# Performance work log

Measured on AMD Instinct MI355X. Metric: run time of the kernel, lower is better.

## Reference

```python
import jax, jax.numpy as jnp
import numpy as np

B, D, N_TYPES = 512, 768, 16
MARGIN = 1.0


def setup_inputs() -> dict:
    key = jax.random.key(0)
    k1, k2 = jax.random.split(key)
    entity_types = jax.random.randint(k1, (B,), 0, N_TYPES, dtype=jnp.int64)
    embeddings = jax.random.normal(k2, (B, D), dtype=jnp.float32)
    return {"entity_types": entity_types, "embeddings": embeddings}


def _pairwise_l2(x):
    # Euclidean distance matrix [B, B], matching torch.cdist(x, x, p=2)
    sq_norm = jnp.sum(x * x, axis=-1)  # [B]
    sq = sq_norm[:, None] + sq_norm[None, :] - 2.0 * (x @ x.T)
    sq = jnp.maximum(sq, 0.0)
    # safe sqrt: zero gradient where sq == 0 (diagonal)
    return jnp.where(sq > 0, jnp.sqrt(jnp.where(sq > 0, sq, 1.0)), 0.0)


def reference(entity_types, embeddings):
    # type_coherence[i, j] = (type_i == type_j)
    type_coherence = entity_types[:, None] == entity_types[None, :]  # [B, B]
    # valid_triplets[a, p, n] = same_type(a, p) & different_type(a, n)
    valid_triplets = type_coherence[:, :, None] & (~type_coherence)[:, None, :]  # [B, B, B]
    distances = _pairwise_l2(embeddings)  # [B, B]
    # triplet_distances[a, p, n] = (d[a, p] - d[a, n]) masked by validity
    triplet_distances = (distances[:, :, None] - distances[:, None, :]) * valid_triplets
    # NOTE: faithful to original — margin added to ALL B^3 entries before clamp,
    # so each invalid triplet contributes clamp(margin, 0) = margin to the sum.
    loss = jnp.sum(jnp.maximum(triplet_distances + MARGIN, 0.0))
    return loss / jnp.sum(valid_triplets)
```

## Files before the change

### kernel.cpp

```cpp
#include <hip/hip_runtime.h>
#include <hip/hip_bf16.h>

#define BSZ 512
#define DIM 768
#define NTYPES 16
#define MARGIN 1.0f
#define PITCH 776

typedef short bf16x8 __attribute__((ext_vector_type(8)));
typedef float f32x4 __attribute__((ext_vector_type(4)));


__global__ __launch_bounds__(256) void gram_kernel(
    const float* __restrict__ emb,
    float* __restrict__ G,
    float* __restrict__ nrm,
    float* __restrict__ out)
{
    const int tid = threadIdx.x;
    const int blk = blockIdx.x;
    const int ti = blk >> 4, tj = blk & 15;
    const int i0 = ti * 32, j0 = tj * 32;

    if (blk == 0 && tid == 0) out[0] = 0.f;

    __shared__ ushort sR[64][PITCH];

    #pragma unroll 12
    for (int it = 0; it < 48; ++it) {
        const int flat = it * 256 + tid;
        const int row = flat / 192;
        const int c4 = flat - row * 192;
        const int grow = (row < 32) ? (i0 + row) : (j0 + row - 32);
        const float4 v = *(const float4*)(emb + (size_t)grow * DIM + c4 * 4);
        __hip_bfloat162 h0 = __float22bfloat162_rn(make_float2(v.x, v.y));
        __hip_bfloat162 h1 = __float22bfloat162_rn(make_float2(v.z, v.w));
        unsigned u0, u1;
        __builtin_memcpy(&u0, &h0, 4);
        __builtin_memcpy(&u1, &h1, 4);
        *(uint2*)&sR[row][c4 * 4] = make_uint2(u0, u1);
    }
    __syncthreads();

    const int lane = tid & 63;
    const int w = tid >> 6;
    const int wr = w >> 1, wc = w & 1;
    const int m = lane & 15;
    const int q = lane >> 4;

    const ushort* arow = &sR[wr * 16 + m][q * 8];
    const ushort* brow = &sR[32 + wc * 16 + m][q * 8];

    f32x4 acc_e = {0.f, 0.f, 0.f, 0.f};
    f32x4 acc_o = {0.f, 0.f, 0.f, 0.f};
    #pragma unroll
    for (int kc = 0; kc < 24; kc += 2) {
        const bf16x8 ae = *(const bf16x8*)(arow + kc * 32);
        const bf16x8 be = *(const bf16x8*)(brow + kc * 32);
        const bf16x8 ao = *(const bf16x8*)(arow + kc * 32 + 32);
        const bf16x8 bo = *(const bf16x8*)(brow + kc * 32 + 32);
        acc_e = __builtin_amdgcn_mfma_f32_16x16x32_bf16(ae, be, acc_e, 0, 0, 0);
        acc_o = __builtin_amdgcn_mfma_f32_16x16x32_bf16(ao, bo, acc_o, 0, 0, 0);
    }

    const int gi = i0 + wr * 16 + 4 * q;
    const int gj = j0 + wc * 16 + m;
    float res[4];
    #pragma unroll
    for (int r = 0; r < 4; ++r) {
        res[r] = acc_e[r] + acc_o[r];
        G[(size_t)(gi + r) * BSZ + gj] = res[r];
    }
    if (ti == tj && wr == wc && (m >> 2) == q)
        nrm[i0 + wr * 16 + m] = res[m & 3];
}

__global__ __launch_bounds__(256) void triplet_kernel(
    const float* __restrict__ G, const float* __restrict__ nrm,
    const int* __restrict__ types, float* __restrict__ out)
{
    const int a = blockIdx.x;
    const int tid = threadIdx.x;
    const int lane = tid & 63;
    const int w = tid >> 6;

    __shared__ float snrm[BSZ];
    __shared__ int   stypes[BSZ];
    __shared__ float pos[BSZ], neg[BSZ];
    __shared__ int   npos, nneg, cnt[NTYPES];
    __shared__ float wsum[4];

    if (tid == 0) { npos = 0; nneg = 0; }
    if (tid < NTYPES) cnt[tid] = 0;
    for (int j = tid; j < BSZ; j += 256) { stypes[j] = types[j]; snrm[j] = nrm[j]; }
    __syncthreads();

    const int ta = stypes[a];
    const float na = snrm[a];
    for (int j = tid; j < BSZ; j += 256) atomicAdd(&cnt[stypes[j]], 1);

    #pragma unroll
    for (int jj = 0; jj < 2; ++jj) {
        const int j = jj * 256 + tid;
        const float g = G[(size_t)a * BSZ + j];
        const float d = sqrtf(fmaxf(na + snrm[j] - 2.f * g, 0.f));
        const bool isp = (stypes[j] == ta);
        const unsigned long long mm = __ballot(isp);
        const unsigned long long below = mm & ((1ull << lane) - 1ull);
        const int cp = __popcll(mm);
        int basep = 0, basen = 0;
        if (lane == 0) {
            basep = atomicAdd(&npos, cp);
            basen = atomicAdd(&nneg, 64 - cp);
        }
        basep = __shfl(basep, 0);
        basen = __shfl(basen, 0);
        const int pb = (int)__popcll(below);
        if (isp) pos[basep + pb] = d;
        else     neg[basen + (lane - pb)] = d;
    }
    __syncthreads();
    const int np = npos, nn = nneg;

    float nr[8];
    #pragma unroll
    for (int c = 0; c < 8; ++c) {
        const int n = c * 64 + lane;
        nr[c] = (n < nn) ? neg[n] : 3.0e38f;
    }
    float local = 0.f;
    for (int pi = w; pi < np; pi += 4) {
        const float dpm = pos[pi] + MARGIN;
        #pragma unroll
        for (int c = 0; c < 8; ++c)
            local += fmaxf(dpm - nr[c], 0.f);
    }

    #pragma unroll
    for (int off = 32; off > 0; off >>= 1) local += __shfl_down(local, off);
    if (lane == 0) wsum[w] = local;
    __syncthreads();
    if (tid == 0) {
        long long V = 0;
        #pragma unroll
        for (int t = 0; t < NTYPES; ++t) {
            long long c = cnt[t];
            V += c * c * (long long)(BSZ - c);
        }
        double bs = (double)wsum[0] + (double)wsum[1]
                  + (double)wsum[2] + (double)wsum[3];
        float contrib = (float)(bs / (double)V);
        if (a == 0) {
            const long long B3 = (long long)BSZ * BSZ * BSZ;
            contrib += (float)((double)(B3 - V) * (double)MARGIN / (double)V);
        }
        atomicAdd(out, contrib);
    }
}

extern "C" void kernel_launch(void* const* d_in, const int* in_sizes, int n_in,
                              void* d_out, int out_size, void* d_ws, size_t ws_size,
                              hipStream_t stream) {
    const int* types = (const int*)d_in[0];
    const float* emb = (const float*)d_in[1];
    float* out = (float*)d_out;

    float* G = (float*)d_ws;
    float* nrm = G + (size_t)BSZ * BSZ;

    gram_kernel<<<256, 256, 0, stream>>>(emb, G, nrm, out);
    triplet_kernel<<<BSZ, 256, 0, stream>>>(G, nrm, types, out);
}
```

Measured before the change: 71.07 us.

## Split-K gram across 8 waves and fuse norm and sqrt into gram kernel

The gram kernel now launches 512 threads and splits the K dimension across two wave groups, which combine their partial sums through shared memory. It computes fp32 row norms while loading the tile and writes the final distance matrix directly, so the separate norm array and the per-element sqrt in the triplet kernel go away. The triplet kernel also issues its distance loads before shared-memory setup to hide their latency. The cost is an extra barrier and shared-memory reduction, and the norms are now computed in fp32 rather than taken from the bf16 diagonal, which changes numerics slightly.

```diff
diff --git a/kernel.cpp b/kernel.cpp
--- a/kernel.cpp
+++ b/kernel.cpp
@@ -6,15 +6,15 @@
 #define NTYPES 16
 #define MARGIN 1.0f
 #define PITCH 776
+#define CPITCH 18
 
 typedef short bf16x8 __attribute__((ext_vector_type(8)));
 typedef float f32x4 __attribute__((ext_vector_type(4)));
 
 
-__global__ __launch_bounds__(256) void gram_kernel(
+__global__ __launch_bounds__(512) void gram_kernel(
     const float* __restrict__ emb,
-    float* __restrict__ G,
-    float* __restrict__ nrm,
+    float* __restrict__ Dm,
     float* __restrict__ out)
 {
     const int tid = threadIdx.x;
@@ -25,26 +25,39 @@
     if (blk == 0 && tid == 0) out[0] = 0.f;
 
     __shared__ ushort sR[64][PITCH];
+    __shared__ float pC[4][16][CPITCH];
+    __shared__ float snrm[64];
 
-    #pragma unroll 12
-    for (int it = 0; it < 48; ++it) {
-        const int flat = it * 256 + tid;
-        const int row = flat / 192;
-        const int c4 = flat - row * 192;
-        const int grow = (row < 32) ? (i0 + row) : (j0 + row - 32);
-        const float4 v = *(const float4*)(emb + (size_t)grow * DIM + c4 * 4);
-        __hip_bfloat162 h0 = __float22bfloat162_rn(make_float2(v.x, v.y));
-        __hip_bfloat162 h1 = __float22bfloat162_rn(make_float2(v.z, v.w));
-        unsigned u0, u1;
-        __builtin_memcpy(&u0, &h0, 4);
-        __builtin_memcpy(&u1, &h1, 4);
-        *(uint2*)&sR[row][c4 * 4] = make_uint2(u0, u1);
+    {
+        const int r = tid >> 3;
+        const int s = tid & 7;
+        const int grow = (r < 32) ? (i0 + r) : (j0 + r - 32);
+        const float* src = emb + (size_t)grow * DIM;
+        float qn = 0.f;
+        #pragma unroll 8
+        for (int it = 0; it < 24; ++it) {
+            const int c4 = s + 8 * it;
+            const float4 v = *(const float4*)(src + c4 * 4);
+            qn += v.x * v.x + v.y * v.y + v.z * v.z + v.w * v.w;
+            __hip_bfloat162 h0 = __float22bfloat162_rn(make_float2(v.x, v.y));
+            __hip_bfloat162 h1 = __float22bfloat162_rn(make_float2(v.z, v.w));
+            unsigned u0, u1;
+            __builtin_memcpy(&u0, &h0, 4);
+            __builtin_memcpy(&u1, &h1, 4);
+            *(uint2*)&sR[r][c4 * 4] = make_uint2(u0, u1);
+        }
+        qn += __shfl_xor(qn, 1);
+        qn += __shfl_xor(qn, 2);
+        qn += __shfl_xor(qn, 4);
+        if (s == 0) snrm[r] = qn;
     }
     __syncthreads();
 
     const int lane = tid & 63;
     const int w = tid >> 6;
-    const int wr = w >> 1, wc = w & 1;
+    const int quad = w & 3;
+    const int kh = w >> 2;
+    const int wr = quad >> 1, wc = quad & 1;
     const int m = lane & 15;
     const int q = lane >> 4;
 
@@ -54,7 +67,8 @@
     f32x4 acc_e = {0.f, 0.f, 0.f, 0.f};
     f32x4 acc_o = {0.f, 0.f, 0.f, 0.f};
     #pragma unroll
-    for (int kc = 0; kc < 24; kc += 2) {
+    for (int u = 0; u < 6; ++u) {
+        const int kc = kh * 12 + 2 * u;
         const bf16x8 ae = *(const bf16x8*)(arow + kc * 32);
         const bf16x8 be = *(const bf16x8*)(brow + kc * 32);
         const bf16x8 ao = *(const bf16x8*)(arow + kc * 32 + 32);
@@ -63,47 +77,56 @@
         acc_o = __builtin_amdgcn_mfma_f32_16x16x32_bf16(ao, bo, acc_o, 0, 0, 0);
     }
 
-    const int gi = i0 + wr * 16 + 4 * q;
-    const int gj = j0 + wc * 16 + m;
-    float res[4];
-    #pragma unroll
-    for (int r = 0; r < 4; ++r) {
-        res[r] = acc_e[r] + acc_o[r];
-        G[(size_t)(gi + r) * BSZ + gj] = res[r];
+    if (kh == 1) {
+        #pragma unroll
+        for (int r = 0; r < 4; ++r)
+            pC[quad][4 * q + r][m] = acc_e[r] + acc_o[r];
     }
-    if (ti == tj && wr == wc && (m >> 2) == q)
-        nrm[i0 + wr * 16 + m] = res[m & 3];
+    __syncthreads();
+
+    if (kh == 0) {
+        const float nj = snrm[32 + wc * 16 + m];
+        #pragma unroll
+        for (int r = 0; r < 4; ++r) {
+            const float g = acc_e[r] + acc_o[r] + pC[quad][4 * q + r][m];
+            const float ni = snrm[wr * 16 + 4 * q + r];
+            Dm[(size_t)(i0 + wr * 16 + 4 * q + r) * BSZ + (j0 + wc * 16 + m)] =
+                sqrtf(fmaxf(ni + nj - 2.f * g, 0.f));
+        }
+    }
 }
 
 __global__ __launch_bounds__(256) void triplet_kernel(
-    const float* __restrict__ G, const float* __restrict__ nrm,
-    const int* __restrict__ types, float* __restrict__ out)
+    const float* __restrict__ Dm, const int* __restrict__ types,
+    float* __restrict__ out)
 {
     const int a = blockIdx.x;
     const int tid = threadIdx.x;
     const int lane = tid & 63;
     const int w = tid >> 6;
 
-    __shared__ float snrm[BSZ];
     __shared__ int   stypes[BSZ];
     __shared__ float pos[BSZ], neg[BSZ];
     __shared__ int   npos, nneg, cnt[NTYPES];
     __shared__ float wsum[4];
 
+    float dval[2];
+    #pragma unroll
+    for (int jj = 0; jj < 2; ++jj)
+        dval[jj] = Dm[(size_t)a * BSZ + jj * 256 + tid];
+
     if (tid == 0) { npos = 0; nneg = 0; }
     if (tid < NTYPES) cnt[tid] = 0;
-    for (int j = tid; j < BSZ; j += 256) { stypes[j] = types[j]; snrm[j] = nrm[j]; }
+    for (int j = tid; j < BSZ; j += 256) stypes[j] = types[j];
     __syncthreads();
 
     const int ta = stypes[a];
-    const float na = snrm[a];
     for (int j = tid; j < BSZ; j += 256) atomicAdd(&cnt[stypes[j]], 1);
 
     #pragma unroll
     for (int jj = 0; jj < 2; ++jj) {
         const int j = jj * 256 + tid;
-        const float g = G[(size_t)a * BSZ + j];
-        const float d = sqrtf(fmaxf(na + snrm[j] - 2.f * g, 0.f));
+        const float d = dval[jj];
         const bool isp = (stypes[j] == ta);
         const unsigned long long mm = __ballot(isp);
         const unsigned long long below = mm & ((1ull << lane) - 1ull);
@@ -165,9 +188,8 @@
     const float* emb = (const float*)d_in[1];
     float* out = (float*)d_out;
 
-    float* G = (float*)d_ws;
-    float* nrm = G + (size_t)BSZ * BSZ;
+    float* Dm = (float*)d_ws;
 
-    gram_kernel<<<256, 256, 0, stream>>>(emb, G, nrm, out);
-    triplet_kernel<<<BSZ, 256, 0, stream>>>(G, nrm, types, out);
+    gram_kernel<<<256, 512, 0, stream>>>(emb, Dm, out);
+    triplet_kernel<<<BSZ, 256, 0, stream>>>(Dm, types, out);
 }
```

Result: faster. 69.51 us (-2.2%).
